# Optimization experiments

Measured on AMD Instinct MI355X. Metric: run time of the kernel, lower is better.

Reference implementation:

```python
import jax, jax.numpy as jnp
import numpy as np

BLOCK_SIZE = 256
RNG_HID = 96
RNG_POS_EMB = 8
TILE_SIZE = 4


def setup_inputs() -> dict:
    out_features = in_features = 4096
    ob, ib = out_features // BLOCK_SIZE, in_features // BLOCK_SIZE
    nb = ob * ib                      # 256 blocks
    tpb = BLOCK_SIZE // TILE_SIZE     # 64 tiles per block side
    key = jax.random.key(0)
    k0, k1, k2, k3, k4 = jax.random.split(key, 5)
    shared_matrix = jax.random.normal(k0, (out_features, in_features), jnp.float32)
    w1 = jax.random.normal(k1, (nb, TILE_SIZE ** 2, RNG_HID), jnp.float32) * (2.0 / RNG_HID) ** 0.5
    b1 = jnp.zeros((nb, RNG_HID), jnp.float32)
    emb_h = jax.random.normal(k2, (nb, tpb, RNG_POS_EMB), jnp.float32) * 0.1
    emb_w = jax.random.normal(k3, (nb, tpb, RNG_POS_EMB), jnp.float32) * 0.1
    shared_matrix_std = (2.0 / (5 * out_features)) ** 0.5
    w2 = jax.random.normal(k4, (nb, RNG_HID, TILE_SIZE ** 2), jnp.float32) * (2.0 / TILE_SIZE ** 2) ** 0.5 * shared_matrix_std
    b2 = jnp.zeros((nb, TILE_SIZE ** 2), jnp.float32)
    scales = jnp.ones((nb, TILE_SIZE ** 2), jnp.float32)
    return {
        'shared_matrix': shared_matrix, 'w1': w1, 'b1': b1,
        'emb_h': emb_h, 'emb_w': emb_w, 'w2': w2, 'b2': b2, 'scales': scales,
    }


def reference(shared_matrix, w1, b1, emb_h, emb_w, w2, b2, scales):
    out_f, in_f = shared_matrix.shape
    ob, ib = out_f // BLOCK_SIZE, in_f // BLOCK_SIZE
    tpb = BLOCK_SIZE // TILE_SIZE
    # tile the matrix: [ob, ib, tpb, tpb, TILE, TILE]
    blocks = shared_matrix.reshape(ob, tpb, TILE_SIZE, ib, tpb, TILE_SIZE).transpose(0, 3, 1, 4, 2, 5)
    flat = blocks.reshape(ob * ib, tpb * tpb, TILE_SIZE * TILE_SIZE)  # [nb, 4096, 16]
    # hypernet layer 1: batched small GEMM, K=16 -> H=96
    hid = jnp.einsum('btk,bkh->bth', flat, w1).reshape(ob * ib, tpb, tpb, RNG_HID)
    hid = hid + b1[:, None, None, :]
    hid = hid.at[:, :, :, :RNG_POS_EMB].add(emb_h[:, :, None, :])          # row positional emb
    hid = hid.at[:, :, :, RNG_POS_EMB:2 * RNG_POS_EMB].add(emb_w[:, None, :, :])  # col positional emb
    hid = jax.nn.elu(hid)
    # hypernet layer 2: H=96 -> 16, plus bias and scaled residual (addcmul)
    out = jnp.einsum('bth,bho->bto', hid.reshape(ob * ib, tpb * tpb, RNG_HID), w2)
    out = out + b2[:, None, :] + flat * scales[:, None, :]
    # untile back to [out_f, in_f]
    out = out.reshape(ob, ib, tpb, tpb, TILE_SIZE, TILE_SIZE).transpose(0, 2, 4, 1, 3, 5).reshape(out_f, in_f)
    return out
```

## Files before the change

kernel.cpp:

```cpp
#include <hip/hip_runtime.h>

#define SM_N 4096

typedef __attribute__((ext_vector_type(8))) short bf16x8;
typedef __attribute__((ext_vector_type(4))) float f32x4;

static __device__ __forceinline__ short f2bf(float f) {
    union { float f; unsigned u; } v; v.f = f;
    return (short)((v.u + 0x7fffu + ((v.u >> 16) & 1u)) >> 16);
}

static __device__ __forceinline__ float elu(float x) {
    return x > 0.0f ? x : (__expf(x) - 1.0f);
}

__global__ __launch_bounds__(256) void adapter_mfma(
    const float* __restrict__ sm,
    const float* __restrict__ w1,
    const float* __restrict__ b1,
    const float* __restrict__ emb_h,
    const float* __restrict__ emb_w,
    const float* __restrict__ w2,
    const float* __restrict__ b2,
    const float* __restrict__ scales,
    float* __restrict__ out)
{
    const int wg   = blockIdx.x;
    const int b    = wg >> 4;
    const int obi  = b >> 4, ibi = b & 15;
    const int tid  = threadIdx.x;
    const int wave = tid >> 6;
    const int lane = tid & 63;
    const int g    = lane >> 4;
    const int ln   = lane & 15;

    const int th = (wg & 15) * 4 + wave;

    const float* __restrict__ w1b = w1 + (size_t)b * 16 * 96;
    const float* __restrict__ w2b = w2 + (size_t)b * 96 * 16;
    const float* __restrict__ b1b = b1 + (size_t)b * 96;
    const float* __restrict__ b2b = b2 + (size_t)b * 16;
    const float* __restrict__ scb = scales + (size_t)b * 16;

    bf16x8 A1[6];
#pragma unroll
    for (int hg = 0; hg < 6; ++hg) {
        bf16x8 a = (bf16x8){0,0,0,0,0,0,0,0};
#pragma unroll
        for (int i = 0; i < 4; ++i)
            a[i] = f2bf(w1b[(4*g + i) * 96 + hg*16 + ln]);
        A1[hg] = a;
    }
    bf16x8 A2[3];
#pragma unroll
    for (int kk = 0; kk < 3; ++kk) {
        bf16x8 a;
#pragma unroll
        for (int i = 0; i < 8; ++i) {
            const int h = 32*kk + 16*(i >> 2) + 4*g + (i & 3);
            a[i] = f2bf(w2b[h * 16 + ln]);
        }
        A2[kk] = a;
    }
    f32x4 B1C[6];
#pragma unroll
    for (int hg = 0; hg < 6; ++hg)
        B1C[hg] = *reinterpret_cast<const f32x4*>(b1b + hg*16 + 4*g);
    const f32x4 b2f = *reinterpret_cast<const f32x4*>(b2b + 4*g);
    const f32x4 scf = *reinterpret_cast<const f32x4*>(scb + 4*g);

    const float* __restrict__ ehp = emb_h + ((size_t)b * 64 + th) * 8 + 4*g;

    const int row0 = obi * 256 + th * 4;
    const float* __restrict__ srow = sm  + (size_t)(row0 + g) * SM_N + ibi * 256 + ln * 4;
    float*       __restrict__ drow = out + (size_t)(row0 + g) * SM_N + ibi * 256 + ln * 4;

#pragma unroll 2
    for (int q = 0; q < 4; ++q) {
        const int tw = q * 16 + ln;
        const f32x4 x4 = *reinterpret_cast<const f32x4*>(srow + q * 64);

        const float* ep = (g < 2) ? ehp
                                  : (emb_w + ((size_t)b * 64 + tw) * 8 + 4*(g - 2));
        const f32x4 ef = *reinterpret_cast<const f32x4*>(ep);

        bf16x8 xb = (bf16x8){0,0,0,0,0,0,0,0};
#pragma unroll
        for (int i = 0; i < 4; ++i) xb[i] = f2bf(x4[i]);

        f32x4 D1[6];
        D1[0] = __builtin_amdgcn_mfma_f32_16x16x32_bf16(A1[0], xb, B1C[0] + ef, 0, 0, 0);
#pragma unroll
        for (int hg = 1; hg < 6; ++hg)
            D1[hg] = __builtin_amdgcn_mfma_f32_16x16x32_bf16(A1[hg], xb, B1C[hg], 0, 0, 0);

        f32x4 acc = b2f + x4 * scf;
#pragma unroll
        for (int kk = 0; kk < 3; ++kk) {
            bf16x8 p;
#pragma unroll
            for (int i = 0; i < 8; ++i)
                p[i] = f2bf(elu(D1[2*kk + (i >> 2)][i & 3]));
            acc = __builtin_amdgcn_mfma_f32_16x16x32_bf16(A2[kk], p, acc, 0, 0, 0);
        }

        *reinterpret_cast<f32x4*>(drow + q * 64) = acc;
    }
}

extern "C" void kernel_launch(void* const* d_in, const int* in_sizes, int n_in,
                              void* d_out, int out_size, void* d_ws, size_t ws_size,
                              hipStream_t stream) {
    const float* sm     = (const float*)d_in[0];
    const float* w1     = (const float*)d_in[1];
    const float* b1     = (const float*)d_in[2];
    const float* emb_h  = (const float*)d_in[3];
    const float* emb_w  = (const float*)d_in[4];
    const float* w2     = (const float*)d_in[5];
    const float* b2     = (const float*)d_in[6];
    const float* scales = (const float*)d_in[7];
    float* out = (float*)d_out;

    adapter_mfma<<<dim3(4096), dim3(256), 0, stream>>>(
        sm, w1, b1, emb_h, emb_w, w2, b2, scales, out);
}
```

Before: 147.6 us.

## Pre-convert hypernet weights to transposed bf16 in a prep kernel

Adds a small prep kernel that converts w1 and w2 to bf16 in a transposed layout in workspace, so each workgroup of the main kernel loads its MFMA A fragments with vector loads instead of many strided scalar loads plus per-element rounding. It also uses packed hardware float-to-bf16 conversion, a med3-based ELU and fma for the residual, and hoists the embedding pointer out of the loop. The cost is an extra kernel launch and a workspace round trip for the weights, which is small next to the 64MB matrix stream.

```diff
diff --git a/kernel.cpp b/kernel.cpp
--- a/kernel.cpp
+++ b/kernel.cpp
@@ -1,28 +1,51 @@
 #include <hip/hip_runtime.h>
+#include <hip/hip_bf16.h>
 
 #define SM_N 4096
 
 typedef __attribute__((ext_vector_type(8))) short bf16x8;
+typedef __attribute__((ext_vector_type(4))) short bf16x4;
 typedef __attribute__((ext_vector_type(4))) float f32x4;
 
-static __device__ __forceinline__ short f2bf(float f) {
-    union { float f; unsigned u; } v; v.f = f;
-    return (short)((v.u + 0x7fffu + ((v.u >> 16) & 1u)) >> 16);
+union Frag8 { bf16x8 v; bf16x4 h[2]; unsigned u[4]; };
+
+static __device__ __forceinline__ unsigned pk2(float lo, float hi) {
+    __hip_bfloat162 t = __float22bfloat162_rn(float2{lo, hi});
+    union { __hip_bfloat162 b; unsigned u; } c; c.b = t;
+    return c.u;
 }
 
 static __device__ __forceinline__ float elu(float x) {
-    return x > 0.0f ? x : (__expf(x) - 1.0f);
+    return __builtin_amdgcn_fmed3f(x, __expf(x) - 1.0f, 0.0f);
+}
+
+__global__ __launch_bounds__(256) void prep_weights(
+    const float* __restrict__ w1, const float* __restrict__ w2,
+    __hip_bfloat16* __restrict__ w1t, __hip_bfloat16* __restrict__ w2t)
+{
+    const int b = blockIdx.x, t = threadIdx.x;
+    const float* __restrict__ w1b = w1 + (size_t)b * 1536;
+    const float* __restrict__ w2b = w2 + (size_t)b * 1536;
+    __hip_bfloat16* __restrict__ o1 = w1t + (size_t)b * 1536;
+    __hip_bfloat16* __restrict__ o2 = w2t + (size_t)b * 1536;
+    const int lo = t & 15, hb = (t >> 4) * 6;
+#pragma unroll
+    for (int i = 0; i < 6; ++i) {
+        const int h = hb + i;
+        o1[h * 16 + lo] = __float2bfloat16(w1b[lo * 96 + h]);
+        o2[lo * 96 + h] = __float2bfloat16(w2b[h * 16 + lo]);
+    }
 }
 
 __global__ __launch_bounds__(256) void adapter_mfma(
     const float* __restrict__ sm,
-    const float* __restrict__ w1,
     const float* __restrict__ b1,
     const float* __restrict__ emb_h,
     const float* __restrict__ emb_w,
-    const float* __restrict__ w2,
     const float* __restrict__ b2,
     const float* __restrict__ scales,
+    const ushort* __restrict__ w1t,
+    const ushort* __restrict__ w2t,
     float* __restrict__ out)
 {
     const int wg   = blockIdx.x;
@@ -33,43 +56,35 @@
     const int lane = tid & 63;
     const int g    = lane >> 4;
     const int ln   = lane & 15;
+    const int th   = (wg & 15) * 4 + wave;
 
-    const int th = (wg & 15) * 4 + wave;
+    const ushort* __restrict__ w1tb = w1t + (size_t)b * 1536;
+    const ushort* __restrict__ w2tb = w2t + (size_t)b * 1536;
 
-    const float* __restrict__ w1b = w1 + (size_t)b * 16 * 96;
-    const float* __restrict__ w2b = w2 + (size_t)b * 96 * 16;
-    const float* __restrict__ b1b = b1 + (size_t)b * 96;
-    const float* __restrict__ b2b = b2 + (size_t)b * 16;
-    const float* __restrict__ scb = scales + (size_t)b * 16;
-
-    bf16x8 A1[6];
+    Frag8 A1[6];
 #pragma unroll
     for (int hg = 0; hg < 6; ++hg) {
-        bf16x8 a = (bf16x8){0,0,0,0,0,0,0,0};
-#pragma unroll
-        for (int i = 0; i < 4; ++i)
-            a[i] = f2bf(w1b[(4*g + i) * 96 + hg*16 + ln]);
-        A1[hg] = a;
+        A1[hg].h[0] = *reinterpret_cast<const bf16x4*>(w1tb + (hg * 16 + ln) * 16 + 4 * g);
+        A1[hg].h[1] = (bf16x4){0, 0, 0, 0};
     }
-    bf16x8 A2[3];
+    Frag8 A2[3];
 #pragma unroll
     for (int kk = 0; kk < 3; ++kk) {
-        bf16x8 a;
-#pragma unroll
-        for (int i = 0; i < 8; ++i) {
-            const int h = 32*kk + 16*(i >> 2) + 4*g + (i & 3);
-            a[i] = f2bf(w2b[h * 16 + ln]);
-        }
-        A2[kk] = a;
+        A2[kk].h[0] = *reinterpret_cast<const bf16x4*>(w2tb + ln * 96 + 32 * kk + 4 * g);
+        A2[kk].h[1] = *reinterpret_cast<const bf16x4*>(w2tb + ln * 96 + 32 * kk + 16 + 4 * g);
     }
+    const float* __restrict__ b1b = b1 + (size_t)b * 96;
     f32x4 B1C[6];
 #pragma unroll
     for (int hg = 0; hg < 6; ++hg)
-        B1C[hg] = *reinterpret_cast<const f32x4*>(b1b + hg*16 + 4*g);
-    const f32x4 b2f = *reinterpret_cast<const f32x4*>(b2b + 4*g);
-    const f32x4 scf = *reinterpret_cast<const f32x4*>(scb + 4*g);
+        B1C[hg] = *reinterpret_cast<const f32x4*>(b1b + hg * 16 + 4 * g);
+    const f32x4 b2f = *reinterpret_cast<const f32x4*>(b2 + (size_t)b * 16 + 4 * g);
+    const f32x4 scf = *reinterpret_cast<const f32x4*>(scales + (size_t)b * 16 + 4 * g);
 
-    const float* __restrict__ ehp = emb_h + ((size_t)b * 64 + th) * 8 + 4*g;
+    const float* __restrict__ ebase = (g < 2)
+        ? emb_h + ((size_t)b * 64 + th) * 8 + 4 * g
+        : emb_w + ((size_t)b * 64 + ln) * 8 + 4 * (g - 2);
+    const int estep = (g < 2) ? 0 : 128;
 
     const int row0 = obi * 256 + th * 4;
     const float* __restrict__ srow = sm  + (size_t)(row0 + g) * SM_N + ibi * 256 + ln * 4;
@@ -77,31 +92,33 @@
 
 #pragma unroll 2
     for (int q = 0; q < 4; ++q) {
-        const int tw = q * 16 + ln;
         const f32x4 x4 = *reinterpret_cast<const f32x4*>(srow + q * 64);
+        const f32x4 ef = *reinterpret_cast<const f32x4*>(ebase + q * estep);
 
-        const float* ep = (g < 2) ? ehp
-                                  : (emb_w + ((size_t)b * 64 + tw) * 8 + 4*(g - 2));
-        const f32x4 ef = *reinterpret_cast<const f32x4*>(ep);
-
-        bf16x8 xb = (bf16x8){0,0,0,0,0,0,0,0};
-#pragma unroll
-        for (int i = 0; i < 4; ++i) xb[i] = f2bf(x4[i]);
+        Frag8 xb;
+        xb.u[0] = pk2(x4[0], x4[1]);
+        xb.u[1] = pk2(x4[2], x4[3]);
+        xb.u[2] = 0; xb.u[3] = 0;
 
         f32x4 D1[6];
-        D1[0] = __builtin_amdgcn_mfma_f32_16x16x32_bf16(A1[0], xb, B1C[0] + ef, 0, 0, 0);
+        D1[0] = __builtin_amdgcn_mfma_f32_16x16x32_bf16(A1[0].v, xb.v, B1C[0] + ef, 0, 0, 0);
 #pragma unroll
         for (int hg = 1; hg < 6; ++hg)
-            D1[hg] = __builtin_amdgcn_mfma_f32_16x16x32_bf16(A1[hg], xb, B1C[hg], 0, 0, 0);
+            D1[hg] = __builtin_amdgcn_mfma_f32_16x16x32_bf16(A1[hg].v, xb.v, B1C[hg], 0, 0, 0);
 
-        f32x4 acc = b2f + x4 * scf;
+        f32x4 acc;
+#pragma unroll
+        for (int i = 0; i < 4; ++i) acc[i] = fmaf(x4[i], scf[i], b2f[i]);
+
 #pragma unroll
         for (int kk = 0; kk < 3; ++kk) {
-            bf16x8 p;
-#pragma unroll
-            for (int i = 0; i < 8; ++i)
-                p[i] = f2bf(elu(D1[2*kk + (i >> 2)][i & 3]));
-            acc = __builtin_amdgcn_mfma_f32_16x16x32_bf16(A2[kk], p, acc, 0, 0, 0);
+            const f32x4 dA = D1[2 * kk], dB = D1[2 * kk + 1];
+            Frag8 p;
+            p.u[0] = pk2(elu(dA[0]), elu(dA[1]));
+            p.u[1] = pk2(elu(dA[2]), elu(dA[3]));
+            p.u[2] = pk2(elu(dB[0]), elu(dB[1]));
+            p.u[3] = pk2(elu(dB[2]), elu(dB[3]));
+            acc = __builtin_amdgcn_mfma_f32_16x16x32_bf16(A2[kk].v, p.v, acc, 0, 0, 0);
         }
 
         *reinterpret_cast<f32x4*>(drow + q * 64) = acc;
@@ -121,6 +138,10 @@
     const float* scales = (const float*)d_in[7];
     float* out = (float*)d_out;
 
+    __hip_bfloat16* w1t = (__hip_bfloat16*)d_ws;
+    __hip_bfloat16* w2t = (__hip_bfloat16*)((char*)d_ws + 786432);
+
+    prep_weights<<<dim3(256), dim3(256), 0, stream>>>(w1, w2, w1t, w2t);
     adapter_mfma<<<dim3(4096), dim3(256), 0, stream>>>(
-        sm, w1, b1, emb_h, emb_w, w2, b2, scales, out);
+        sm, b1, emb_h, emb_w, b2, scales, (const ushort*)w1t, (const ushort*)w2t, out);
 }
```

New measurement: 151.2 us. 1.02x slower.
